# Performance work log

Measured on AMD Instinct MI355X. Metric: run time of the kernel, lower is better.

The kernel has to match this reference:

```python
import jax, jax.numpy as jnp
import numpy as np

B_SZ, L, D_MODEL = 8, 200, 256
D_STATE, D_CONV, N_BANDS = 64, 4, 4
D_INNER = 2 * D_MODEL
DT_RANK = -(-D_MODEL // 16)  # ceil(d_model/16) = 16
EPS = 1e-12


def setup_inputs() -> dict:
    key = jax.random.key(0)
    ks = jax.random.split(key, 12)
    s = lambda k, shape, scale: jax.random.normal(k, shape, jnp.float32) * scale
    return {
        "x": s(ks[0], (B_SZ, L, D_MODEL), 1.0),
        "cos_phi": s(ks[1], (B_SZ, N_BANDS, L), 1.0),
        "sin_phi": s(ks[2], (B_SZ, N_BANDS, L), 1.0),
        "delta_mag": jax.random.uniform(ks[3], (B_SZ, N_BANDS, L), jnp.float32),
        "W_in": s(ks[4], (D_MODEL, 2 * D_INNER), D_MODEL ** -0.5),
        "conv_w": s(ks[5], (D_INNER, 1, D_CONV), 0.5),
        "conv_b": jnp.zeros((D_INNER,), jnp.float32),
        "W_x": s(ks[6], (D_INNER, DT_RANK + 2 * D_STATE), D_INNER ** -0.5),
        "W_dt": s(ks[7], (DT_RANK, D_INNER), DT_RANK ** -0.5),
        "b_dt": jnp.zeros((D_INNER,), jnp.float32),
        "A_log": jnp.log(jnp.tile(jnp.arange(1, D_STATE + 1, dtype=jnp.float32), (D_INNER, 1))),
        "D_skip": jnp.ones((D_INNER,), jnp.float32),
        "W_out": s(ks[8], (D_INNER, D_MODEL), D_INNER ** -0.5),
        "gamma": jnp.ones((D_MODEL,), jnp.float32),
        "beta": jnp.zeros((D_MODEL,), jnp.float32),
        "W_phase": s(ks[9], (2 * N_BANDS, D_STATE), (2 * N_BANDS) ** -0.5),
    }


def _selective_scan(u, dt, A, B_st, C_st):
    # u, dt: [B,L,Di]; A: [Di,N]; B_st, C_st: [B,L,N]
    dA = jnp.exp(jnp.einsum('bld,dn->bldn', dt, A))          # [B,L,Di,N]
    dBu = jnp.einsum('bld,bln->bldn', dt, B_st) * u[..., None]  # [B,L,Di,N]

    def step(h, inputs):
        dA_t, dBu_t, C_t = inputs
        h = dA_t * h + dBu_t                                  # [B,Di,N]
        y = jnp.einsum('bdn,bn->bd', h, C_t)                  # [B,Di]
        return h, y

    h0 = jnp.zeros((u.shape[0], u.shape[2], A.shape[1]), u.dtype)
    xs = (jnp.swapaxes(dA, 0, 1), jnp.swapaxes(dBu, 0, 1), jnp.swapaxes(C_st, 0, 1))
    _, ys = jax.lax.scan(step, h0, xs)                        # ys: [L,B,Di]
    return jnp.swapaxes(ys, 0, 1)


def reference(x, cos_phi, sin_phi, delta_mag, W_in, conv_w, conv_b, W_x, W_dt, b_dt,
              A_log, D_skip, W_out, gamma, beta, W_phase):
    residual = x
    xz = x @ W_in                                             # [B,L,2*Di]
    x_m, z = jnp.split(xz, 2, axis=-1)

    # causal depthwise conv1d: torch pads both sides with d_conv-1 then trims to L,
    # equivalent to left-pad (d_conv-1) + valid conv
    xc = jnp.swapaxes(x_m, 1, 2)                              # [B,Di,L]
    xc = jax.lax.conv_general_dilated(
        xc, conv_w, window_strides=(1,), padding=[(D_CONV - 1, 0)],
        dimension_numbers=('NCH', 'OIH', 'NCH'), feature_group_count=D_INNER)
    xc = xc + conv_b[None, :, None]
    x_m = jax.nn.silu(jnp.swapaxes(xc, 1, 2))                 # [B,L,Di]

    xp = x_m @ W_x
    dt_lr = xp[..., :DT_RANK]
    B_st = xp[..., DT_RANK:DT_RANK + D_STATE]
    C_st = xp[..., DT_RANK + D_STATE:]

    dt = jax.nn.softplus(dt_lr @ W_dt + b_dt)                 # [B,L,Di]
    dmm = jnp.mean(delta_mag, axis=1)[..., None]              # [B,L,1]
    dt = dt * (1.0 + jax.nn.softplus(dmm))

    phase_feats = jnp.swapaxes(jnp.concatenate([cos_phi, sin_phi], axis=1), 1, 2)  # [B,L,2*n_bands]
    C_st = C_st + phase_feats @ W_phase

    A = -jnp.exp(A_log)
    y = _selective_scan(x_m, dt, A, B_st, C_st)
    y = y + x_m * D_skip
    y = y * jax.nn.silu(z)
    out = y @ W_out + residual

    mu = jnp.mean(out, axis=-1, keepdims=True)
    var = jnp.mean((out - mu) ** 2, axis=-1, keepdims=True)
    return (out - mu) * jax.lax.rsqrt(var + EPS) * gamma + beta
```

## Files before the change

kernel.cpp:

```cpp
#include <hip/hip_runtime.h>
#include <hip/hip_bf16.h>

#define B_SZ 8
#define LSEQ 200
#define DMODEL 256
#define DINNER 512
#define DSTATE 64
#define DTRANK 16
#define ROWS (B_SZ * LSEQ)

using bf16x8 = __attribute__((ext_vector_type(8))) short;
using f32x4  = __attribute__((ext_vector_type(4))) float;

__device__ __forceinline__ float softplusf(float x) {
    return (x > 20.f) ? x : log1pf(__expf(x));
}
__device__ __forceinline__ float siluf(float x) {
    return x / (1.f + __expf(-x));
}
__device__ __forceinline__ unsigned short f2bf(float f) {
    union { float f; unsigned int u; } v; v.f = f;
    unsigned int r = v.u + 0x7FFF + ((v.u >> 16) & 1);
    return (unsigned short)(r >> 16);
}
__device__ __forceinline__ float bf2f(unsigned short u) {
    union { unsigned int i; float f; } v;
    v.i = ((unsigned int)u) << 16;
    return v.f;
}

__global__ __launch_bounds__(256) void prep_w_k(
    const float* __restrict__ x, const float* __restrict__ W_in,
    const float* __restrict__ W_x, const float* __restrict__ W_out,
    unsigned short* __restrict__ x_hi,  unsigned short* __restrict__ x_lo,
    unsigned short* __restrict__ WiT_hi, unsigned short* __restrict__ WiT_lo,
    unsigned short* __restrict__ WxT_hi, unsigned short* __restrict__ WxT_lo,
    unsigned short* __restrict__ WoT_hi, unsigned short* __restrict__ WoT_lo)
{
    int idx = blockIdx.x * 256 + threadIdx.x;
    float v;
    unsigned short *dh, *dl;
    size_t di;
    if (idx < 409600) {
        v = x[idx]; dh = x_hi; dl = x_lo; di = idx;
    } else if (idx < 409600 + 262144) {
        int l = idx - 409600;
        int n = l >> 8, k = l & 255;
        v = W_in[(size_t)k * 1024 + n]; dh = WiT_hi; dl = WiT_lo; di = l;
    } else if (idx < 409600 + 262144 + 73728) {
        int l = idx - (409600 + 262144);
        int n = l >> 9, k = l & 511;
        v = W_x[(size_t)k * 144 + n]; dh = WxT_hi; dl = WxT_lo; di = l;
    } else if (idx < 409600 + 262144 + 73728 + 131072) {
        int l = idx - (409600 + 262144 + 73728);
        int n = l >> 9, k = l & 511;
        v = W_out[(size_t)k * 256 + n]; dh = WoT_hi; dl = WoT_lo; di = l;
    } else return;
    unsigned short h = f2bf(v);
    dh[di] = h;
    dl[di] = f2bf(v - bf2f(h));
}

__global__ __launch_bounds__(256) void gemm_mfma(
    const unsigned short* __restrict__ A_hi, const unsigned short* __restrict__ A_lo,
    const unsigned short* __restrict__ BT_hi, const unsigned short* __restrict__ BT_lo,
    float* __restrict__ C, int M, int N, int K, const float* __restrict__ resid)
{
    __shared__ unsigned short As_hi[64 * 40], As_lo[64 * 40];
    __shared__ unsigned short Bs_hi[64 * 40], Bs_lo[64 * 40];

    const int t    = threadIdx.x;
    const int m0   = blockIdx.y * 64;
    const int n0   = blockIdx.x * 64;
    const int lane = t & 63;
    const int w    = t >> 6;
    const int wm   = (w >> 1) * 32;
    const int wn   = (w & 1) * 32;
    const int fr   = lane & 15;
    const int fq   = lane >> 4;

    const int sr = t >> 2;
    const int sc = (t & 3) * 8;

    f32x4 acc[2][2] = {};

    const size_t a_off = (size_t)(m0 + sr) * K + sc;
    const int    brow  = n0 + sr;
    const size_t b_off = (size_t)brow * K + sc;
    const bool   bok   = brow < N;

    for (int k0 = 0; k0 < K; k0 += 32) {
        int4 ah = *(const int4*)(A_hi + a_off + k0);
        int4 al = *(const int4*)(A_lo + a_off + k0);
        int4 bh = make_int4(0, 0, 0, 0), bl = make_int4(0, 0, 0, 0);
        if (bok) {
            bh = *(const int4*)(BT_hi + b_off + k0);
            bl = *(const int4*)(BT_lo + b_off + k0);
        }
        __syncthreads();
        *(int4*)&As_hi[sr * 40 + sc] = ah;
        *(int4*)&As_lo[sr * 40 + sc] = al;
        *(int4*)&Bs_hi[sr * 40 + sc] = bh;
        *(int4*)&Bs_lo[sr * 40 + sc] = bl;
        __syncthreads();

        bf16x8 a_h[2], a_l[2], b_h[2], b_l[2];
#pragma unroll
        for (int mi = 0; mi < 2; mi++) {
            int row = wm + mi * 16 + fr;
            a_h[mi] = *(const bf16x8*)&As_hi[row * 40 + fq * 8];
            a_l[mi] = *(const bf16x8*)&As_lo[row * 40 + fq * 8];
        }
#pragma unroll
        for (int ni = 0; ni < 2; ni++) {
            int row = wn + ni * 16 + fr;
            b_h[ni] = *(const bf16x8*)&Bs_hi[row * 40 + fq * 8];
            b_l[ni] = *(const bf16x8*)&Bs_lo[row * 40 + fq * 8];
        }
#pragma unroll
        for (int mi = 0; mi < 2; mi++)
#pragma unroll
            for (int ni = 0; ni < 2; ni++) {
                acc[mi][ni] = __builtin_amdgcn_mfma_f32_16x16x32_bf16(a_h[mi], b_h[ni], acc[mi][ni], 0, 0, 0);
                acc[mi][ni] = __builtin_amdgcn_mfma_f32_16x16x32_bf16(a_h[mi], b_l[ni], acc[mi][ni], 0, 0, 0);
                acc[mi][ni] = __builtin_amdgcn_mfma_f32_16x16x32_bf16(a_l[mi], b_h[ni], acc[mi][ni], 0, 0, 0);
            }
    }

#pragma unroll
    for (int mi = 0; mi < 2; mi++)
#pragma unroll
        for (int ni = 0; ni < 2; ni++) {
            int col = n0 + wn + ni * 16 + fr;
            if (col < N) {
#pragma unroll
                for (int reg = 0; reg < 4; reg++) {
                    int row = m0 + wm + mi * 16 + fq * 4 + reg;
                    float v = acc[mi][ni][reg];
                    if (resid) v += resid[(size_t)row * N + col];
                    C[(size_t)row * N + col] = v;
                }
            }
        }
}

__global__ __launch_bounds__(256) void conv_silu_k(
    const float* __restrict__ xz, const float* __restrict__ conv_w,
    const float* __restrict__ conv_b, float* __restrict__ xm,
    unsigned short* __restrict__ xm_hi, unsigned short* __restrict__ xm_lo)
{
    int idx = blockIdx.x * 256 + threadIdx.x;
    int c = idx & 511;
    int r = idx >> 9;
    int l = r % LSEQ;

    float w0 = conv_w[c * 4 + 0];
    float w1 = conv_w[c * 4 + 1];
    float w2 = conv_w[c * 4 + 2];
    float w3 = conv_w[c * 4 + 3];

    const float* base = xz + (size_t)r * 1024 + c;
    float acc = conv_b[c];
    if (l >= 3) acc = fmaf(base[-3 * 1024], w0, acc);
    if (l >= 2) acc = fmaf(base[-2 * 1024], w1, acc);
    if (l >= 1) acc = fmaf(base[-1 * 1024], w2, acc);
    acc = fmaf(base[0], w3, acc);

    float s = siluf(acc);
    xm[idx] = s;
    unsigned short h = f2bf(s);
    xm_hi[idx] = h;
    xm_lo[idx] = f2bf(s - bf2f(h));
}

__global__ __launch_bounds__(256) void pack_bc_k(
    const float* __restrict__ cosp, const float* __restrict__ sinp,
    const float* __restrict__ W_phase, const float* __restrict__ xp,
    float* __restrict__ bcp)
{
    int idx = blockIdx.x * 256 + threadIdx.x;
    int n = idx & 63;
    int r = idx >> 6;
    int b = r / LSEQ, l = r % LSEQ;

    float acc = 0.f;
#pragma unroll
    for (int j = 0; j < 4; j++) {
        float cp = cosp[(b * 4 + j) * LSEQ + l];
        float sp = sinp[(b * 4 + j) * LSEQ + l];
        acc = fmaf(cp, W_phase[j * 64 + n], acc);
        acc = fmaf(sp, W_phase[(4 + j) * 64 + n], acc);
    }
    float Bv = xp[(size_t)r * 144 + 16 + n];
    float Cv = xp[(size_t)r * 144 + 80 + n] + acc;
    *(float2*)&bcp[(size_t)r * 128 + 2 * n] = make_float2(Bv, Cv);
}

__global__ __launch_bounds__(256) void dt_k(
    const float* __restrict__ xp, const float* __restrict__ W_dt,
    const float* __restrict__ b_dt, const float* __restrict__ dmag,
    const float* __restrict__ xm, float2* __restrict__ dtpack)
{
    int r = blockIdx.x;
    int t = threadIdx.x;
    int b = r / LSEQ, l = r % LSEQ;

    __shared__ float xr[16];
    __shared__ float sscale;
    if (t < 16) xr[t] = xp[(size_t)r * 144 + t];
    if (t == 16) {
        float dm = 0.f;
#pragma unroll
        for (int j = 0; j < 4; j++)
            dm += dmag[(b * 4 + j) * LSEQ + l];
        dm *= 0.25f;
        sscale = 1.f + softplusf(dm);
    }
    __syncthreads();
    float scale = sscale;

#pragma unroll
    for (int rep = 0; rep < 2; rep++) {
        int d = t + rep * 256;
        float acc = b_dt[d];
#pragma unroll
        for (int i = 0; i < 16; i++)
            acc = fmaf(xr[i], W_dt[i * 512 + d], acc);
        float dtv = softplusf(acc) * scale;
        float u = xm[(size_t)r * 512 + d];
        dtpack[(size_t)r * 512 + d] = make_float2(dtv, dtv * u);
    }
}

__global__ __launch_bounds__(256, 4) void scan_k(
    const float2* __restrict__ dtpack, const float* __restrict__ bcp,
    const float* __restrict__ xm, const float* __restrict__ xz,
    const float* __restrict__ A_log, const float* __restrict__ D_skip,
    unsigned short* __restrict__ yf_hi, unsigned short* __restrict__ yf_lo)
{
    int wv0  = blockIdx.x * 4 + (threadIdx.x >> 6);
    int wv   = __builtin_amdgcn_readfirstlane(wv0);
    int lane = threadIdx.x & 63;
    int b = wv >> 9;
    int d = wv & 511;

    float A  = -__expf(A_log[d * 64 + lane]);
    float Dd = D_skip[d];

    const float2* dtp = dtpack + (size_t)b * LSEQ * 512 + d;
    const float*  bcr = bcp + (size_t)b * LSEQ * 128 + 2 * lane;
    const float*  xmb = xm  + (size_t)b * LSEQ * 512 + d;
    const float*  xzb = xz  + (size_t)b * LSEQ * 1024 + 512 + d;
    unsigned short* yph = yf_hi + (size_t)b * LSEQ * 512 + d;
    unsigned short* ypl = yf_lo + (size_t)b * LSEQ * 512 + d;

    const bool lo32 = (lane & 32) == 0;
    const bool lo16 = (lane & 16) == 0;
    const bool lo8  = (lane & 8)  == 0;
    const bool store_lane = (lane & 7) == 0;
    const int  tsel = lane >> 3;

    float h = 0.f;

    float2 bcA[8], bcB[8], dqA[8], dqB[8];
    float uA, zA, uB, zB;

#define PREF(BC, DQ, L0)                                        \
    _Pragma("unroll")                                           \
    for (int t = 0; t < 8; t++) {                               \
        BC[t] = *(const float2*)&bcr[((L0) + t) * 128];         \
        DQ[t] = dtp[((L0) + t) * 512];                          \
    }

#define UZ(U, Z, L0)                                            \
    {                                                           \
        U = 0.f; Z = 0.f;                                       \
        if (store_lane) {                                       \
            int lu = (L0) + tsel;                               \
            U = xmb[lu * 512];                                  \
            Z = xzb[lu * 1024];                                 \
        }                                                       \
    }

#define STEP(BC, DQ, U, Z, L0)                                  \
    {                                                           \
        float p[8];                                             \
        _Pragma("unroll")                                       \
        for (int t = 0; t < 8; t++) {                           \
            float e = __expf(DQ[t].x * A);                      \
            h = fmaf(e, h, DQ[t].y * BC[t].x);                  \
            p[t] = h * BC[t].y;                                 \
        }                                                       \
        float q[4];                                             \
        _Pragma("unroll")                                       \
        for (int i = 0; i < 4; i++) {                           \
            float keep = lo32 ? p[i] : p[i + 4];                \
            float send = lo32 ? p[i + 4] : p[i];                \
            q[i] = keep + __shfl_xor(send, 32, 64);             \
        }                                                       \
        float r2[2];                                            \
        _Pragma("unroll")                                       \
        for (int i = 0; i < 2; i++) {                           \
            float keep = lo16 ? q[i] : q[i + 2];                \
            float send = lo16 ? q[i + 2] : q[i];                \
            r2[i] = keep + __shfl_xor(send, 16, 64);            \
        }                                                       \
        float keepf = lo8 ? r2[0] : r2[1];                      \
        float sendf = lo8 ? r2[1] : r2[0];                      \
        float s = keepf + __shfl_xor(sendf, 8, 64);             \
        s += __shfl_xor(s, 4, 64);                              \
        s += __shfl_xor(s, 2, 64);                              \
        s += __shfl_xor(s, 1, 64);                              \
        if (store_lane) {                                       \
            int lu = (L0) + tsel;                               \
            float yv = (s + (U) * Dd) * siluf(Z);               \
            unsigned short hh = f2bf(yv);                       \
            yph[lu * 512] = hh;                                 \
            ypl[lu * 512] = f2bf(yv - bf2f(hh));                \
        }                                                       \
    }

    PREF(bcA, dqA, 0);
    int l0 = 0;
#pragma unroll 1
    for (int it = 0; it < 12; it++) {
        UZ(uA, zA, l0);
        PREF(bcB, dqB, l0 + 8);
        STEP(bcA, dqA, uA, zA, l0);
        UZ(uB, zB, l0 + 8);
        PREF(bcA, dqA, l0 + 16);
        STEP(bcB, dqB, uB, zB, l0 + 8);
        l0 += 16;
    }
    UZ(uA, zA, 192);
    STEP(bcA, dqA, uA, zA, 192);

#undef PREF
#undef UZ
#undef STEP
}

__global__ __launch_bounds__(256) void ln_k(
    const float* __restrict__ outp, const float* __restrict__ gamma,
    const float* __restrict__ beta, float* __restrict__ out)
{
    int r = blockIdx.x;
    int t = threadIdx.x;
    float v = outp[(size_t)r * 256 + t];
    float s = v, ss = v * v;
#pragma unroll
    for (int off = 32; off > 0; off >>= 1) {
        s  += __shfl_xor(s,  off, 64);
        ss += __shfl_xor(ss, off, 64);
    }
    __shared__ float red[8];
    int w = t >> 6;
    if ((t & 63) == 0) { red[w] = s; red[4 + w] = ss; }
    __syncthreads();
    s  = red[0] + red[1] + red[2] + red[3];
    ss = red[4] + red[5] + red[6] + red[7];
    float mu  = s * (1.f / 256.f);
    float var = ss * (1.f / 256.f) - mu * mu;
    if (var < 0.f) var = 0.f;
    float inv = rsqrtf(var + 1e-12f);
    float o = (v - mu) * inv * gamma[t] + beta[t];
    out[(size_t)r * 256 + t] = o;
}

extern "C" void kernel_launch(void* const* d_in, const int* in_sizes, int n_in,
                              void* d_out, int out_size, void* d_ws, size_t ws_size,
                              hipStream_t stream)
{
    const float* x       = (const float*)d_in[0];
    const float* cosp    = (const float*)d_in[1];
    const float* sinp    = (const float*)d_in[2];
    const float* dmag    = (const float*)d_in[3];
    const float* W_in    = (const float*)d_in[4];
    const float* conv_w  = (const float*)d_in[5];
    const float* conv_b  = (const float*)d_in[6];
    const float* W_x     = (const float*)d_in[7];
    const float* W_dt    = (const float*)d_in[8];
    const float* b_dt    = (const float*)d_in[9];
    const float* A_log   = (const float*)d_in[10];
    const float* D_skip  = (const float*)d_in[11];
    const float* W_out   = (const float*)d_in[12];
    const float* gamma   = (const float*)d_in[13];
    const float* beta    = (const float*)d_in[14];
    const float* W_phase = (const float*)d_in[15];
    float* out = (float*)d_out;

    char* ws = (char*)d_ws;
    float*  xz     = (float*)ws;  ws += (size_t)ROWS * 1024 * 4;
    float*  xm     = (float*)ws;  ws += (size_t)ROWS * 512 * 4;
    float*  xp     = (float*)ws;  ws += (size_t)ROWS * 144 * 4;
    float*  bcp    = (float*)ws;  ws += (size_t)ROWS * 128 * 4;
    float2* dtpack = (float2*)ws; ws += (size_t)ROWS * 512 * 8;
    float*  outp   = (float*)ws;  ws += (size_t)ROWS * 256 * 4;
    unsigned short* x_hi   = (unsigned short*)ws; ws += (size_t)ROWS * 256 * 2;
    unsigned short* x_lo   = (unsigned short*)ws; ws += (size_t)ROWS * 256 * 2;
    unsigned short* WiT_hi = (unsigned short*)ws; ws += (size_t)1024 * 256 * 2;
    unsigned short* WiT_lo = (unsigned short*)ws; ws += (size_t)1024 * 256 * 2;
    unsigned short* WxT_hi = (unsigned short*)ws; ws += (size_t)144 * 512 * 2;
    unsigned short* WxT_lo = (unsigned short*)ws; ws += (size_t)144 * 512 * 2;
    unsigned short* WoT_hi = (unsigned short*)ws; ws += (size_t)256 * 512 * 2;
    unsigned short* WoT_lo = (unsigned short*)ws; ws += (size_t)256 * 512 * 2;
    unsigned short* xm_hi  = (unsigned short*)ws; ws += (size_t)ROWS * 512 * 2;
    unsigned short* xm_lo  = (unsigned short*)ws; ws += (size_t)ROWS * 512 * 2;
    unsigned short* yf_hi  = (unsigned short*)ws; ws += (size_t)ROWS * 512 * 2;
    unsigned short* yf_lo  = (unsigned short*)ws; ws += (size_t)ROWS * 512 * 2;

    dim3 blk(256);
    prep_w_k   <<<dim3(3424),   blk, 0, stream>>>(x, W_in, W_x, W_out,
                                                  x_hi, x_lo, WiT_hi, WiT_lo,
                                                  WxT_hi, WxT_lo, WoT_hi, WoT_lo);
    gemm_mfma  <<<dim3(16, 25), blk, 0, stream>>>(x_hi, x_lo, WiT_hi, WiT_lo,
                                                  xz, ROWS, 1024, 256, nullptr);
    conv_silu_k<<<dim3(3200),   blk, 0, stream>>>(xz, conv_w, conv_b, xm, xm_hi, xm_lo);
    gemm_mfma  <<<dim3(3, 25),  blk, 0, stream>>>(xm_hi, xm_lo, WxT_hi, WxT_lo,
                                                  xp, ROWS, 144, 512, nullptr);
    pack_bc_k  <<<dim3(400),    blk, 0, stream>>>(cosp, sinp, W_phase, xp, bcp);
    dt_k       <<<dim3(1600),   blk, 0, stream>>>(xp, W_dt, b_dt, dmag, xm, dtpack);
    scan_k     <<<dim3(1024),   blk, 0, stream>>>(dtpack, bcp, xm, xz, A_log, D_skip,
                                                  yf_hi, yf_lo);
    gemm_mfma  <<<dim3(4, 25),  blk, 0, stream>>>(yf_hi, yf_lo, WoT_hi, WoT_lo,
                                                  outp, ROWS, 256, 512, x);
    ln_k       <<<dim3(1600),   blk, 0, stream>>>(outp, gamma, beta, out);
}
```

Baseline: 180.3 us.

## Transpose dt pack to per-channel layout, swizzle scan blocks, use exp2

The dt kernel now processes a batch and a 64-channel slice per block. It stages results in shared memory and writes them transposed, so each scan wave reads its channel's dt/dt*u sequence contiguously as float4. Before, those loads were strided by 512 per timestep. The scan also remaps block indices so neighbouring blocks cover different channel groups, and it replaces __expf with a raw exp2 using a prescaled A. The dt kernel shrinks to 64 blocks, which risks poor occupancy for that stage.

```diff
diff --git a/kernel.cpp b/kernel.cpp
--- a/kernel.cpp
+++ b/kernel.cpp
@@ -196,58 +196,97 @@
     *(float2*)&bcp[(size_t)r * 128 + 2 * n] = make_float2(Bv, Cv);
 }
 
-__global__ __launch_bounds__(256) void dt_k(
+__global__ __launch_bounds__(256) void dtprep_k(
     const float* __restrict__ xp, const float* __restrict__ W_dt,
     const float* __restrict__ b_dt, const float* __restrict__ dmag,
-    const float* __restrict__ xm, float2* __restrict__ dtpack)
-{
-    int r = blockIdx.x;
-    int t = threadIdx.x;
-    int b = r / LSEQ, l = r % LSEQ;
-
-    __shared__ float xr[16];
-    __shared__ float sscale;
-    if (t < 16) xr[t] = xp[(size_t)r * 144 + t];
-    if (t == 16) {
+    const float* __restrict__ xm, float2* __restrict__ dtpackT)
+{
+    __shared__ float xr[LSEQ * 17];
+    __shared__ float scl[LSEQ];
+    __shared__ float2 dtb[64][65];
+
+    const int t  = threadIdx.x;
+    const int b  = blockIdx.x >> 3;
+    const int d0 = (blockIdx.x & 7) * 64;
+    const int dd = t & 63;
+    const int lg = t >> 6;
+
+    for (int idx = t; idx < LSEQ * 16; idx += 256) {
+        int l = idx >> 4, i = idx & 15;
+        xr[l * 17 + i] = xp[(size_t)(b * LSEQ + l) * 144 + i];
+    }
+    if (t < LSEQ) {
         float dm = 0.f;
 #pragma unroll
         for (int j = 0; j < 4; j++)
-            dm += dmag[(b * 4 + j) * LSEQ + l];
-        dm *= 0.25f;
-        sscale = 1.f + softplusf(dm);
-    }
+            dm += dmag[(b * 4 + j) * LSEQ + t];
+        scl[t] = 1.f + softplusf(dm * 0.25f);
+    }
+
+    float wreg[16];
+#pragma unroll
+    for (int i = 0; i < 16; i++)
+        wreg[i] = W_dt[i * 512 + d0 + dd];
+    float bb = b_dt[d0 + dd];
+
     __syncthreads();
-    float scale = sscale;
-
-#pragma unroll
-    for (int rep = 0; rep < 2; rep++) {
-        int d = t + rep * 256;
-        float acc = b_dt[d];
-#pragma unroll
-        for (int i = 0; i < 16; i++)
-            acc = fmaf(xr[i], W_dt[i * 512 + d], acc);
-        float dtv = softplusf(acc) * scale;
-        float u = xm[(size_t)r * 512 + d];
-        dtpack[(size_t)r * 512 + d] = make_float2(dtv, dtv * u);
+
+    for (int c = 0; c < 4; c++) {
+#pragma unroll 1
+        for (int j = 0; j < 16; j++) {
+            int lloc = lg * 16 + j;
+            int l = c * 64 + lloc;
+            if (l < LSEQ) {
+                float acc = bb;
+#pragma unroll
+                for (int i = 0; i < 16; i++)
+                    acc = fmaf(xr[l * 17 + i], wreg[i], acc);
+                float dtv = softplusf(acc) * scl[l];
+                float u = xm[(size_t)(b * LSEQ + l) * 512 + d0 + dd];
+                dtb[dd][lloc] = make_float2(dtv, dtv * u);
+            }
+        }
+        __syncthreads();
+        {
+            int dd_o = t >> 2;
+            int lo16 = (t & 3) * 16;
+#pragma unroll
+            for (int i = 0; i < 16; i += 2) {
+                int l = c * 64 + lo16 + i;
+                if (l + 1 < LSEQ + 1 && l < LSEQ) {
+                    float2 a0 = dtb[dd_o][lo16 + i];
+                    float2 a1 = dtb[dd_o][lo16 + i + 1];
+                    if (l + 1 < LSEQ) {
+                        float4 v = make_float4(a0.x, a0.y, a1.x, a1.y);
+                        *(float4*)&dtpackT[(size_t)(b * 512 + d0 + dd_o) * LSEQ + l] = v;
+                    } else {
+                        dtpackT[(size_t)(b * 512 + d0 + dd_o) * LSEQ + l] = a0;
+                    }
+                }
+            }
+        }
+        __syncthreads();
     }
 }
 
 __global__ __launch_bounds__(256, 4) void scan_k(
-    const float2* __restrict__ dtpack, const float* __restrict__ bcp,
+    const float2* __restrict__ dtpackT, const float* __restrict__ bcp,
     const float* __restrict__ xm, const float* __restrict__ xz,
     const float* __restrict__ A_log, const float* __restrict__ D_skip,
     unsigned short* __restrict__ yf_hi, unsigned short* __restrict__ yf_lo)
 {
-    int wv0  = blockIdx.x * 4 + (threadIdx.x >> 6);
+    int bid  = blockIdx.x;
+    int swz  = (bid & 7) * 128 + (bid >> 3);
+    int wv0  = swz * 4 + (threadIdx.x >> 6);
     int wv   = __builtin_amdgcn_readfirstlane(wv0);
     int lane = threadIdx.x & 63;
     int b = wv >> 9;
     int d = wv & 511;
 
-    float A  = -__expf(A_log[d * 64 + lane]);
+    float A2 = -__expf(A_log[d * 64 + lane]) * 1.4426950408889634f;
     float Dd = D_skip[d];
 
-    const float2* dtp = dtpack + (size_t)b * LSEQ * 512 + d;
+    const float4* dtp4 = (const float4*)(dtpackT + (size_t)(b * 512 + d) * LSEQ);
     const float*  bcr = bcp + (size_t)b * LSEQ * 128 + 2 * lane;
     const float*  xmb = xm  + (size_t)b * LSEQ * 512 + d;
     const float*  xzb = xz  + (size_t)b * LSEQ * 1024 + 512 + d;
@@ -262,15 +301,17 @@
 
     float h = 0.f;
 
-    float2 bcA[8], bcB[8], dqA[8], dqB[8];
+    float2 bcA[8], bcB[8];
+    float4 dqA[4], dqB[4];
     float uA, zA, uB, zB;
 
 #define PREF(BC, DQ, L0)                                        \
     _Pragma("unroll")                                           \
-    for (int t = 0; t < 8; t++) {                               \
+    for (int t = 0; t < 8; t++)                                 \
         BC[t] = *(const float2*)&bcr[((L0) + t) * 128];         \
-        DQ[t] = dtp[((L0) + t) * 512];                          \
-    }
+    _Pragma("unroll")                                           \
+    for (int j = 0; j < 4; j++)                                 \
+        DQ[j] = dtp4[((L0) >> 1) + j];
 
 #define UZ(U, Z, L0)                                            \
     {                                                           \
@@ -287,8 +328,10 @@
         float p[8];                                             \
         _Pragma("unroll")                                       \
         for (int t = 0; t < 8; t++) {                           \
-            float e = __expf(DQ[t].x * A);                      \
-            h = fmaf(e, h, DQ[t].y * BC[t].x);                  \
+            float dtv = ((t & 1) == 0) ? DQ[t >> 1].x : DQ[t >> 1].z; \
+            float dtu = ((t & 1) == 0) ? DQ[t >> 1].y : DQ[t >> 1].w; \
+            float e = __builtin_amdgcn_exp2f(dtv * A2);         \
+            h = fmaf(e, h, dtu * BC[t].x);                      \
             p[t] = h * BC[t].y;                                 \
         }                                                       \
         float q[4];                                             \
@@ -419,7 +462,7 @@
     gemm_mfma  <<<dim3(3, 25),  blk, 0, stream>>>(xm_hi, xm_lo, WxT_hi, WxT_lo,
                                                   xp, ROWS, 144, 512, nullptr);
     pack_bc_k  <<<dim3(400),    blk, 0, stream>>>(cosp, sinp, W_phase, xp, bcp);
-    dt_k       <<<dim3(1600),   blk, 0, stream>>>(xp, W_dt, b_dt, dmag, xm, dtpack);
+    dtprep_k   <<<dim3(64),     blk, 0, stream>>>(xp, W_dt, b_dt, dmag, xm, dtpack);
     scan_k     <<<dim3(1024),   blk, 0, stream>>>(dtpack, bcp, xm, xz, A_log, D_skip,
                                                   yf_hi, yf_lo);
     gemm_mfma  <<<dim3(4, 25),  blk, 0, stream>>>(yf_hi, yf_lo, WoT_hi, WoT_lo,
```

After: 216.3 us. 1.2x slower.
